# Optimization experiments

Hardware: AMD Instinct MI355X
Metric: run time of the kernel (lower is better)

## Reference

```python
import jax, jax.numpy as jnp
import numpy as np

EMBED_DIM = 1024
NUM_HEADS = 16
HEAD_DIM = EMBED_DIM // NUM_HEADS
THRESHOLD = 0.001
B, S = 8, 1024


def setup_inputs() -> dict:
    key = jax.random.key(0)
    ks = jax.random.split(key, 7)
    sc = 1.0 / np.sqrt(EMBED_DIM)
    return {
        "x": jax.random.normal(ks[0], (B, S, EMBED_DIM), dtype=jnp.float32),
        "Wq": jax.random.normal(ks[1], (NUM_HEADS, EMBED_DIM, HEAD_DIM), dtype=jnp.float32) * sc,
        "bq": jax.random.normal(ks[2], (NUM_HEADS, HEAD_DIM), dtype=jnp.float32) * 0.01,
        "Wk": jax.random.normal(ks[3], (NUM_HEADS, EMBED_DIM, HEAD_DIM), dtype=jnp.float32) * sc,
        "bk": jax.random.normal(ks[4], (NUM_HEADS, HEAD_DIM), dtype=jnp.float32) * 0.01,
        "Wv": jax.random.normal(ks[5], (NUM_HEADS, EMBED_DIM, HEAD_DIM), dtype=jnp.float32) * sc,
        "bv": jax.random.normal(ks[6], (NUM_HEADS, HEAD_DIM), dtype=jnp.float32) * 0.01,
    }


def thresholded_softmax(scores, threshold):
    # softmax over last dim, zero entries below threshold, renormalize
    s = jax.nn.softmax(scores, axis=-1)
    s = jnp.where(s < threshold, 0.0, s)
    return s / (jnp.sum(s, axis=-1, keepdims=True) + 1e-12)


def reference(x, Wq, bq, Wk, bk, Wv, bv):
    # x: [B,S,D]; Wq/Wk/Wv: [H,D,e]; biases: [H,e]
    scale = jnp.asarray(EMBED_DIM ** 0.5, x.dtype)  # note: scales by sqrt(embed_dim), not head_dim
    Q = jnp.einsum("bsd,hde->hbse", x, Wq) + bq[:, None, None, :]
    K = jnp.einsum("bsd,hde->hbse", x, Wk) + bk[:, None, None, :]
    V = jnp.einsum("bsd,hde->hbse", x, Wv) + bv[:, None, None, :]
    scores = jnp.einsum("hbse,hbte->hbst", Q, K) / scale  # [H,B,S,S]
    att = thresholded_softmax(scores, THRESHOLD)
    latent = jnp.einsum("hbst,hbte->hbse", att, V)  # [H,B,S,e]
    # concat heads along last dim in head order -> [B,S,H*e]
    residual = jnp.transpose(latent, (1, 2, 0, 3)).reshape(x.shape[0], x.shape[1], -1)
    x_res = x + residual  # dropout p=0.0 -> identity
    return (x_res, att)
```

## Files before the change

### kernel.cpp

```cpp
#include <hip/hip_runtime.h>
#include <hip/hip_bf16.h>
#include <cstdint>
#include <cstddef>

#define B_ 8
#define S_ 1024
#define H_ 16
#define E_ 64
#define D_ 1024

typedef unsigned short u16;
typedef short s16x8 __attribute__((ext_vector_type(8)));
typedef float f32x4 __attribute__((ext_vector_type(4)));

__device__ __forceinline__ u16 f2b(float f) {
  union { float f; unsigned u; } v; v.f = f;
  unsigned u = v.u;
  return (u16)((u + 0x7FFFu + ((u >> 16) & 1u)) >> 16);
}

__device__ __forceinline__ void gload16(const void* g, void* lds) {
  __builtin_amdgcn_global_load_lds(
      (const __attribute__((address_space(1))) void*)g,
      (__attribute__((address_space(3))) void*)lds, 16, 0, 0);
}

#define BARL() do {                                          \
  asm volatile("s_waitcnt lgkmcnt(0)" ::: "memory");         \
  __builtin_amdgcn_sched_barrier(0);                         \
  __builtin_amdgcn_s_barrier();                              \
  __builtin_amdgcn_sched_barrier(0);                         \
  asm volatile("" ::: "memory");                             \
} while (0)

__global__ void k_prep(const float* __restrict__ x, u16* __restrict__ xb,
                       const float* __restrict__ Wq, const float* __restrict__ Wk,
                       const float* __restrict__ Wv, u16* __restrict__ wbt) {
  if (blockIdx.x < 4096) {
    size_t i = ((size_t)blockIdx.x * 256 + threadIdx.x) * 8;
    float4 a = *(const float4*)(x + i);
    float4 b = *(const float4*)(x + i + 4);
    uint4 o;
    o.x = f2b(a.x) | ((unsigned)f2b(a.y) << 16);
    o.y = f2b(a.z) | ((unsigned)f2b(a.w) << 16);
    o.z = f2b(b.x) | ((unsigned)f2b(b.y) << 16);
    o.w = f2b(b.z) | ((unsigned)f2b(b.w) << 16);
    *(uint4*)(xb + i) = o;
    return;
  }
  __shared__ u16 T[64][65];
  int bid = blockIdx.x - 4096;
  int d0 = (bid & 15) * 64;
  int mh = bid >> 4;
  int mat = mh >> 4, h = mh & 15;
  const float* W = (mat == 0) ? Wq : (mat == 1) ? Wk : Wv;
  int tid = threadIdx.x;
#pragma unroll
  for (int rep = 0; rep < 4; rep++) {
    int dl = rep * 16 + (tid >> 4);
    int e0 = (tid & 15) * 4;
    float4 v = *(const float4*)(W + (size_t)h * (D_ * E_) + (size_t)(d0 + dl) * E_ + e0);
    T[dl][e0] = f2b(v.x); T[dl][e0 + 1] = f2b(v.y);
    T[dl][e0 + 2] = f2b(v.z); T[dl][e0 + 3] = f2b(v.w);
  }
  __syncthreads();
#pragma unroll
  for (int rep = 0; rep < 4; rep++) {
    int el = rep * 16 + (tid >> 4);
    int dl0 = (tid & 15) * 4;
    ushort4 o;
    o.x = T[dl0][el]; o.y = T[dl0 + 1][el]; o.z = T[dl0 + 2][el]; o.w = T[dl0 + 3][el];
    int n = mat * 1024 + h * 64 + el;
    *(ushort4*)(wbt + (size_t)n * D_ + d0 + dl0) = o;
  }
}

__global__ __launch_bounds__(256) void k_qkv(
    const u16* __restrict__ xb, const u16* __restrict__ wbt,
    const float* __restrict__ bq, const float* __restrict__ bk, const float* __restrict__ bv,
    u16* __restrict__ Qb, u16* __restrict__ Kb, u16* __restrict__ Vt) {
  __shared__ u16 As[128 * 64];
  __shared__ u16 Bs[128 * 64];
  int tid = threadIdx.x, l = tid & 63, w = tid >> 6;
  int bid = blockIdx.x;
  int xcd = bid & 7, i = bid >> 3;
  int m0 = (xcd * 8 + i / 24) * 128;
  int n0 = (i % 24) * 128;
  int wm = w >> 1, wn = w & 1;
  int rl = l & 15, kg = l >> 4;
  f32x4 acc[4][4] = {};
  for (int k0 = 0; k0 < D_; k0 += 64) {
#pragma unroll
    for (int i2 = 0; i2 < 4; i2++) {
      int ci = w * 4 + i2;
      int r = ci * 8 + (l >> 3);
      int c = (l & 7) ^ (r & 7);
      gload16(xb  + (size_t)(m0 + r) * D_ + k0 + c * 8, (char*)As + ci * 1024);
      gload16(wbt + (size_t)(n0 + r) * D_ + k0 + c * 8, (char*)Bs + ci * 1024);
    }
    __syncthreads();
#pragma unroll
    for (int kk = 0; kk < 2; kk++) {
      s16x8 af[4], bfr[4];
      int chunk = kk * 4 + kg;
#pragma unroll
      for (int fm = 0; fm < 4; fm++) {
        int r = wm * 64 + fm * 16 + rl;
        af[fm] = *(const s16x8*)(As + r * 64 + ((chunk ^ (r & 7)) * 8));
      }
#pragma unroll
      for (int fn = 0; fn < 4; fn++) {
        int r = wn * 64 + fn * 16 + rl;
        bfr[fn] = *(const s16x8*)(Bs + r * 64 + ((chunk ^ (r & 7)) * 8));
      }
#pragma unroll
      for (int fm = 0; fm < 4; fm++)
#pragma unroll
        for (int fn = 0; fn < 4; fn++)
          acc[fm][fn] = __builtin_amdgcn_mfma_f32_16x16x32_bf16(af[fm], bfr[fn], acc[fm][fn], 0, 0, 0);
    }
    __syncthreads();
  }
#pragma unroll
  for (int fn = 0; fn < 4; fn++) {
    int n = n0 + wn * 64 + fn * 16 + rl;
    int mat = n >> 10, h = (n >> 6) & 15, e = n & 63;
    const float* bias = (mat == 0) ? bq : (mat == 1) ? bk : bv;
    float bval = bias[h * 64 + e];
    if (mat == 2) {
#pragma unroll
      for (int fm = 0; fm < 4; fm++) {
        int sq = m0 + wm * 64 + fm * 16 + kg * 4;
        int bb = sq >> 10, s = sq & 1023;
        ushort4 o;
        o.x = f2b(acc[fm][fn][0] + bval);
        o.y = f2b(acc[fm][fn][1] + bval);
        o.z = f2b(acc[fm][fn][2] + bval);
        o.w = f2b(acc[fm][fn][3] + bval);
        *(ushort4*)(Vt + ((size_t)((h * B_ + bb) * E_ + e) << 10) + s) = o;
      }
    } else {
      u16* dst = (mat == 0) ? Qb : Kb;
#pragma unroll
      for (int fm = 0; fm < 4; fm++)
#pragma unroll
        for (int j = 0; j < 4; j++) {
          int m = m0 + wm * 64 + fm * 16 + kg * 4 + j;
          int bb = m >> 10, s = m & 1023;
          dst[(size_t)((h * B_ + bb) * S_ + s) * E_ + e] = f2b(acc[fm][fn][j] + bval);
        }
    }
  }
}

__global__ __launch_bounds__(512, 2) void f_attn(
    const u16* __restrict__ Qb, const u16* __restrict__ Kb, const u16* __restrict__ Vt,
    const float* __restrict__ x, float* __restrict__ att, float* __restrict__ out) {
  __shared__ u16 Qlds[64 * 64];
  __shared__ u16 KV[1024 * 64];
  __shared__ u16 Ab[2][64 * 64];
  __shared__ float red[3][64][4];

  int p = blockIdx.x;
  int L = (p & 7) * 256 + (p >> 3);
  int hb = L >> 4, mblk = L & 15;
  int m0 = mblk * 64;
  int tid = threadIdx.x, l = tid & 63, w = tid >> 6;
  int rl = l & 15, kg = l >> 4;
  int rh = w >> 2, cq = w & 3;

  const u16* Qp = Qb + (size_t)hb * (S_ * E_) + (size_t)m0 * E_;
  const u16* Kp = Kb + (size_t)hb * (S_ * E_);
  const u16* Vp = Vt + (size_t)hb * (S_ * E_);

  {
    int r = w * 8 + (l >> 3), c = (l & 7) ^ (r & 7);
    gload16(Qp + (size_t)r * E_ + c * 8, (char*)Qlds + w * 1024);
  }
#pragma unroll
  for (int i = 0; i < 16; i++) {
    int ci = w * 16 + i;
    int r = ci * 8 + (l >> 3), c = (l & 7) ^ (r & 7);
    gload16(Kp + (size_t)r * E_ + c * 8, (char*)KV + ci * 1024);
  }
  __syncthreads();

  s16x8 af[2][2];
#pragma unroll
  for (int fm = 0; fm < 2; fm++)
#pragma unroll
    for (int kk = 0; kk < 2; kk++) {
      int r = rh * 32 + fm * 16 + rl, ch = kk * 4 + kg;
      af[fm][kk] = *(const s16x8*)((const char*)Qlds + r * 128 + ((ch ^ (r & 7)) * 16));
    }

  f32x4 acc[2][16];
#pragma unroll
  for (int fm = 0; fm < 2; fm++)
#pragma unroll
    for (int ct = 0; ct < 16; ct++)
#pragma unroll
      for (int j = 0; j < 4; j++) acc[fm][ct][j] = 0.f;

#pragma unroll
  for (int ct = 0; ct < 16; ct++) {
    s16x8 bf[2];
#pragma unroll
    for (int kk = 0; kk < 2; kk++) {
      int r = ct * 64 + cq * 16 + rl, ch = kk * 4 + kg;
      bf[kk] = *(const s16x8*)((const char*)KV + r * 128 + ((ch ^ (r & 7)) * 16));
    }
#pragma unroll
    for (int fm = 0; fm < 2; fm++)
#pragma unroll
      for (int kk = 0; kk < 2; kk++)
        acc[fm][ct] = __builtin_amdgcn_mfma_f32_16x16x32_bf16(af[fm][kk], bf[kk], acc[fm][ct], 0, 0, 0);
  }
  __syncthreads();

#pragma unroll
  for (int i = 0; i < 16; i++) {
    int ci = w * 16 + i;
    int e = ci >> 1, hf = ci & 1;
    int c = ((hf * 64 + l) & ~7) | ((l & 7) ^ (e & 7));
    gload16(Vp + (size_t)e * S_ + c * 8, (char*)KV + e * 2048 + hf * 1024);
  }

  int mh2 = w >> 1, nh2 = w & 1;
  int h = hb >> 3, bb = hb & 7;
  float xv[2][4];
#pragma unroll
  for (int fn = 0; fn < 2; fn++)
#pragma unroll
    for (int j = 0; j < 4; j++) {
      int mq = m0 + mh2 * 16 + kg * 4 + j;
      int e = h * 64 + nh2 * 32 + fn * 16 + rl;
      xv[fn][j] = x[(((size_t)bb * S_ + mq) << 10) + e];
    }

  float mx[2][4], Z[2][4], Z2[2][4];
#pragma unroll
  for (int fm = 0; fm < 2; fm++)
#pragma unroll
    for (int j = 0; j < 4; j++) {
      float m = acc[fm][0][j];
#pragma unroll
      for (int ct = 1; ct < 16; ct++) m = fmaxf(m, acc[fm][ct][j]);
#pragma unroll
      for (int off = 8; off >= 1; off >>= 1) m = fmaxf(m, __shfl_xor(m, off));
      mx[fm][j] = m;
    }
  if (rl == 0) {
#pragma unroll
    for (int fm = 0; fm < 2; fm++)
#pragma unroll
      for (int j = 0; j < 4; j++) red[0][rh * 32 + fm * 16 + kg * 4 + j][cq] = mx[fm][j];
  }
  BARL();
#pragma unroll
  for (int fm = 0; fm < 2; fm++)
#pragma unroll
    for (int j = 0; j < 4; j++) {
      f32x4 r4 = *(const f32x4*)&red[0][rh * 32 + fm * 16 + kg * 4 + j][0];
      mx[fm][j] = fmaxf(fmaxf(r4[0], r4[1]), fmaxf(r4[2], r4[3]));
    }
#pragma unroll
  for (int fm = 0; fm < 2; fm++)
#pragma unroll
    for (int j = 0; j < 4; j++) {
      float s = 0.f;
#pragma unroll
      for (int ct = 0; ct < 16; ct++) {
        float e = __expf((acc[fm][ct][j] - mx[fm][j]) * 0.03125f);
        acc[fm][ct][j] = e;
        s += e;
      }
#pragma unroll
      for (int off = 8; off >= 1; off >>= 1) s += __shfl_xor(s, off);
      Z[fm][j] = s;
    }
  if (rl == 0) {
#pragma unroll
    for (int fm = 0; fm < 2; fm++)
#pragma unroll
      for (int j = 0; j < 4; j++) red[1][rh * 32 + fm * 16 + kg * 4 + j][cq] = Z[fm][j];
  }
  BARL();
#pragma unroll
  for (int fm = 0; fm < 2; fm++)
#pragma unroll
    for (int j = 0; j < 4; j++) {
      f32x4 r4 = *(const f32x4*)&red[1][rh * 32 + fm * 16 + kg * 4 + j][0];
      Z[fm][j] = r4[0] + r4[1] + r4[2] + r4[3];
    }
#pragma unroll
  for (int fm = 0; fm < 2; fm++)
#pragma unroll
    for (int j = 0; j < 4; j++) {
      float thr = 0.001f * Z[fm][j];
      float s = 0.f;
#pragma unroll
      for (int ct = 0; ct < 16; ct++) {
        float e = acc[fm][ct][j];
        e = (e >= thr) ? e : 0.f;
        acc[fm][ct][j] = e;
        s += e;
      }
#pragma unroll
      for (int off = 8; off >= 1; off >>= 1) s += __shfl_xor(s, off);
      Z2[fm][j] = s;
    }
  if (rl == 0) {
#pragma unroll
    for (int fm = 0; fm < 2; fm++)
#pragma unroll
      for (int j = 0; j < 4; j++) red[2][rh * 32 + fm * 16 + kg * 4 + j][cq] = Z2[fm][j];
  }
  BARL();
#pragma unroll
  for (int fm = 0; fm < 2; fm++)
#pragma unroll
    for (int j = 0; j < 4; j++) {
      f32x4 r4 = *(const f32x4*)&red[2][rh * 32 + fm * 16 + kg * 4 + j][0];
      float z2 = r4[0] + r4[1] + r4[2] + r4[3];
      float inv = 1.f / (z2 + 1e-12f * Z[fm][j]);
#pragma unroll
      for (int ct = 0; ct < 16; ct++) acc[fm][ct][j] *= inv;
    }

  asm volatile("s_waitcnt vmcnt(0)" ::: "memory");
  __builtin_amdgcn_sched_barrier(0);

  float* attp = att + ((size_t)hb << 20) + ((size_t)m0 << 10);
#pragma unroll
  for (int fm = 0; fm < 2; fm++)
#pragma unroll
    for (int j = 0; j < 4; j++) {
      int m = rh * 32 + fm * 16 + kg * 4 + j;
#pragma unroll
      for (int ct = 0; ct < 16; ct++)
        attp[((size_t)m << 10) + ct * 64 + cq * 16 + rl] = acc[fm][ct][j];
    }

  f32x4 acc2[2];
#pragma unroll
  for (int fn = 0; fn < 2; fn++)
#pragma unroll
    for (int j = 0; j < 4; j++) acc2[fn][j] = 0.f;

#pragma unroll
  for (int fm = 0; fm < 2; fm++)
#pragma unroll
    for (int j = 0; j < 4; j++) {
      int m = rh * 32 + fm * 16 + kg * 4 + j;
      int tl = cq * 16 + rl;
      *(u16*)((char*)Ab[0] + m * 128 + (((tl >> 3) ^ (m & 7)) * 16) + (tl & 7) * 2)
          = f2b(acc[fm][0][j]);
    }
  BARL();

#pragma unroll
  for (int ct = 0; ct < 16; ct++) {
    s16x8 a2[2], b2[2][2];
#pragma unroll
    for (int kk = 0; kk < 2; kk++) {
      int ch = kk * 4 + kg;
      int rA = mh2 * 16 + rl;
      a2[kk] = *(const s16x8*)((const char*)Ab[ct & 1] + rA * 128 + ((ch ^ (rA & 7)) * 16));
#pragma unroll
      for (int fn = 0; fn < 2; fn++) {
        int e = nh2 * 32 + fn * 16 + rl;
        b2[fn][kk] = *(const s16x8*)((const char*)KV + e * 2048 + ct * 128 + ((ch ^ (e & 7)) * 16));
      }
    }
    if (ct < 15) {
#pragma unroll
      for (int fm = 0; fm < 2; fm++)
#pragma unroll
        for (int j = 0; j < 4; j++) {
          int m = rh * 32 + fm * 16 + kg * 4 + j;
          int tl = cq * 16 + rl;
          *(u16*)((char*)Ab[(ct + 1) & 1] + m * 128 + (((tl >> 3) ^ (m & 7)) * 16) + (tl & 7) * 2)
              = f2b(acc[fm][ct + 1][j]);
        }
    }
    __builtin_amdgcn_s_setprio(1);
#pragma unroll
    for (int fn = 0; fn < 2; fn++)
#pragma unroll
      for (int kk = 0; kk < 2; kk++)
        acc2[fn] = __builtin_amdgcn_mfma_f32_16x16x32_bf16(a2[kk], b2[fn][kk], acc2[fn], 0, 0, 0);
    __builtin_amdgcn_s_setprio(0);
    BARL();
  }

#pragma unroll
  for (int fn = 0; fn < 2; fn++)
#pragma unroll
    for (int j = 0; j < 4; j++) {
      int mq = m0 + mh2 * 16 + kg * 4 + j;
      int e = h * 64 + nh2 * 32 + fn * 16 + rl;
      size_t idx = (((size_t)bb * S_ + mq) << 10) + e;
      out[idx] = xv[fn][j] + acc2[fn][j];
    }
}

extern "C" void kernel_launch(void* const* d_in, const int* in_sizes, int n_in,
                              void* d_out, int out_size, void* d_ws, size_t ws_size,
                              hipStream_t stream) {
  const float* x  = (const float*)d_in[0];
  const float* Wq = (const float*)d_in[1];
  const float* bq = (const float*)d_in[2];
  const float* Wk = (const float*)d_in[3];
  const float* bk = (const float*)d_in[4];
  const float* Wv = (const float*)d_in[5];
  const float* bv = (const float*)d_in[6];
  float* xres = (float*)d_out;
  float* att  = xres + (size_t)B_ * S_ * D_;

  char* ws = (char*)d_ws;
  u16* xb  = (u16*)(ws);
  u16* wbt = (u16*)(ws + 16777216);
  u16* Qb  = (u16*)(ws + 23068672);
  u16* Kb  = (u16*)(ws + 39845888);
  u16* Vt  = (u16*)(ws + 56623104);

  k_prep  <<<dim3(4864), dim3(256), 0, stream>>>(x, xb, Wq, Wk, Wv, wbt);
  k_qkv   <<<dim3(1536), dim3(256), 0, stream>>>(xb, wbt, bq, bk, bv, Qb, Kb, Vt);
  f_attn  <<<dim3(2048), dim3(512), 0, stream>>>(Qb, Kb, Vt, x, att, xres);
}
```

Before: 287.9 us.

## Shrink attention tile to 32 rows and stream K/V in halves

The attention kernel now processes 32 query rows per block with 4 waves (256 threads) instead of 64 rows with 8 waves. It loads K and V in two 512-column halves into a smaller LDS buffer, which cuts LDS use so more blocks can be resident per CU. It also moves the att write after the PV loop and doubles the grid. In exchange, each block re-reads K/V from global or L2 twice as often per query row, and the extra sync points on the half-loads can stall.

```diff
diff --git a/kernel.cpp b/kernel.cpp
--- a/kernel.cpp
+++ b/kernel.cpp
@@ -153,21 +153,20 @@
   }
 }
 
-__global__ __launch_bounds__(512, 2) void f_attn(
+__global__ __launch_bounds__(256, 2) void f_attn(
     const u16* __restrict__ Qb, const u16* __restrict__ Kb, const u16* __restrict__ Vt,
     const float* __restrict__ x, float* __restrict__ att, float* __restrict__ out) {
-  __shared__ u16 Qlds[64 * 64];
-  __shared__ u16 KV[1024 * 64];
-  __shared__ u16 Ab[2][64 * 64];
-  __shared__ float red[3][64][4];
+  __shared__ u16 KV[512 * 64];
+  __shared__ u16 Ab[2][32 * 64];
+  __shared__ u16 Qlds[32 * 64];
+  __shared__ float red[3][32][4];
 
   int p = blockIdx.x;
-  int L = (p & 7) * 256 + (p >> 3);
-  int hb = L >> 4, mblk = L & 15;
-  int m0 = mblk * 64;
+  int L = (p & 7) * 512 + (p >> 3);
+  int hb = L >> 5, mblk = L & 31;
+  int m0 = mblk * 32;
   int tid = threadIdx.x, l = tid & 63, w = tid >> 6;
   int rl = l & 15, kg = l >> 4;
-  int rh = w >> 2, cq = w & 3;
 
   const u16* Qp = Qb + (size_t)hb * (S_ * E_) + (size_t)m0 * E_;
   const u16* Kp = Kb + (size_t)hb * (S_ * E_);
@@ -190,8 +189,8 @@
   for (int fm = 0; fm < 2; fm++)
 #pragma unroll
     for (int kk = 0; kk < 2; kk++) {
-      int r = rh * 32 + fm * 16 + rl, ch = kk * 4 + kg;
-      af[fm][kk] = *(const s16x8*)((const char*)Qlds + r * 128 + ((ch ^ (r & 7)) * 16));
+      int q = fm * 16 + rl, ch = kk * 4 + kg;
+      af[fm][kk] = *(const s16x8*)((const char*)Qlds + q * 128 + ((ch ^ (q & 7)) * 16));
     }
 
   f32x4 acc[2][16];
@@ -203,11 +202,11 @@
       for (int j = 0; j < 4; j++) acc[fm][ct][j] = 0.f;
 
 #pragma unroll
-  for (int ct = 0; ct < 16; ct++) {
+  for (int ct = 0; ct < 8; ct++) {
     s16x8 bf[2];
 #pragma unroll
     for (int kk = 0; kk < 2; kk++) {
-      int r = ct * 64 + cq * 16 + rl, ch = kk * 4 + kg;
+      int r = ct * 64 + w * 16 + rl, ch = kk * 4 + kg;
       bf[kk] = *(const s16x8*)((const char*)KV + r * 128 + ((ch ^ (r & 7)) * 16));
     }
 #pragma unroll
@@ -216,26 +215,48 @@
       for (int kk = 0; kk < 2; kk++)
         acc[fm][ct] = __builtin_amdgcn_mfma_f32_16x16x32_bf16(af[fm][kk], bf[kk], acc[fm][ct], 0, 0, 0);
   }
-  __syncthreads();
+  BARL();
 
 #pragma unroll
   for (int i = 0; i < 16; i++) {
     int ci = w * 16 + i;
-    int e = ci >> 1, hf = ci & 1;
-    int c = ((hf * 64 + l) & ~7) | ((l & 7) ^ (e & 7));
-    gload16(Vp + (size_t)e * S_ + c * 8, (char*)KV + e * 2048 + hf * 1024);
-  }
-
-  int mh2 = w >> 1, nh2 = w & 1;
+    int r = ci * 8 + (l >> 3), c = (l & 7) ^ (r & 7);
+    gload16(Kp + (size_t)(512 + r) * E_ + c * 8, (char*)KV + ci * 1024);
+  }
+  __syncthreads();
+
+#pragma unroll
+  for (int ct = 0; ct < 8; ct++) {
+    s16x8 bf[2];
+#pragma unroll
+    for (int kk = 0; kk < 2; kk++) {
+      int r = ct * 64 + w * 16 + rl, ch = kk * 4 + kg;
+      bf[kk] = *(const s16x8*)((const char*)KV + r * 128 + ((ch ^ (r & 7)) * 16));
+    }
+#pragma unroll
+    for (int fm = 0; fm < 2; fm++)
+#pragma unroll
+      for (int kk = 0; kk < 2; kk++)
+        acc[fm][8 + ct] = __builtin_amdgcn_mfma_f32_16x16x32_bf16(af[fm][kk], bf[kk], acc[fm][8 + ct], 0, 0, 0);
+  }
+  BARL();
+
+#pragma unroll
+  for (int i = 0; i < 16; i++) {
+    int e = w * 16 + i;
+    int c = (l & ~7) | ((l & 7) ^ (e & 7));
+    gload16(Vp + (size_t)e * S_ + c * 8, (char*)KV + e * 1024);
+  }
+
   int h = hb >> 3, bb = hb & 7;
   float xv[2][4];
 #pragma unroll
-  for (int fn = 0; fn < 2; fn++)
-#pragma unroll
-    for (int j = 0; j < 4; j++) {
-      int mq = m0 + mh2 * 16 + kg * 4 + j;
-      int e = h * 64 + nh2 * 32 + fn * 16 + rl;
-      xv[fn][j] = x[(((size_t)bb * S_ + mq) << 10) + e];
+  for (int fm = 0; fm < 2; fm++)
+#pragma unroll
+    for (int j = 0; j < 4; j++) {
+      int mq = m0 + fm * 16 + kg * 4 + j;
+      int e = h * 64 + w * 16 + rl;
+      xv[fm][j] = x[(((size_t)bb * S_ + mq) << 10) + e];
     }
 
   float mx[2][4], Z[2][4], Z2[2][4];
@@ -254,14 +275,14 @@
 #pragma unroll
     for (int fm = 0; fm < 2; fm++)
 #pragma unroll
-      for (int j = 0; j < 4; j++) red[0][rh * 32 + fm * 16 + kg * 4 + j][cq] = mx[fm][j];
-  }
-  BARL();
-#pragma unroll
-  for (int fm = 0; fm < 2; fm++)
-#pragma unroll
-    for (int j = 0; j < 4; j++) {
-      f32x4 r4 = *(const f32x4*)&red[0][rh * 32 + fm * 16 + kg * 4 + j][0];
+      for (int j = 0; j < 4; j++) red[0][fm * 16 + kg * 4 + j][w] = mx[fm][j];
+  }
+  BARL();
+#pragma unroll
+  for (int fm = 0; fm < 2; fm++)
+#pragma unroll
+    for (int j = 0; j < 4; j++) {
+      f32x4 r4 = *(const f32x4*)&red[0][fm * 16 + kg * 4 + j][0];
       mx[fm][j] = fmaxf(fmaxf(r4[0], r4[1]), fmaxf(r4[2], r4[3]));
     }
 #pragma unroll
@@ -283,14 +304,14 @@
 #pragma unroll
     for (int fm = 0; fm < 2; fm++)
 #pragma unroll
-      for (int j = 0; j < 4; j++) red[1][rh * 32 + fm * 16 + kg * 4 + j][cq] = Z[fm][j];
-  }
-  BARL();
-#pragma unroll
-  for (int fm = 0; fm < 2; fm++)
-#pragma unroll
-    for (int j = 0; j < 4; j++) {
-      f32x4 r4 = *(const f32x4*)&red[1][rh * 32 + fm * 16 + kg * 4 + j][0];
+      for (int j = 0; j < 4; j++) red[1][fm * 16 + kg * 4 + j][w] = Z[fm][j];
+  }
+  BARL();
+#pragma unroll
+  for (int fm = 0; fm < 2; fm++)
+#pragma unroll
+    for (int j = 0; j < 4; j++) {
+      f32x4 r4 = *(const f32x4*)&red[1][fm * 16 + kg * 4 + j][0];
       Z[fm][j] = r4[0] + r4[1] + r4[2] + r4[3];
     }
 #pragma unroll
@@ -314,14 +335,14 @@
 #pragma unroll
     for (int fm = 0; fm < 2; fm++)
 #pragma unroll
-      for (int j = 0; j < 4; j++) red[2][rh * 32 + fm * 16 + kg * 4 + j][cq] = Z2[fm][j];
-  }
-  BARL();
-#pragma unroll
-  for (int fm = 0; fm < 2; fm++)
-#pragma unroll
-    for (int j = 0; j < 4; j++) {
-      f32x4 r4 = *(const f32x4*)&red[2][rh * 32 + fm * 16 + kg * 4 + j][0];
+      for (int j = 0; j < 4; j++) red[2][fm * 16 + kg * 4 + j][w] = Z2[fm][j];
+  }
+  BARL();
+#pragma unroll
+  for (int fm = 0; fm < 2; fm++)
+#pragma unroll
+    for (int j = 0; j < 4; j++) {
+      f32x4 r4 = *(const f32x4*)&red[2][fm * 16 + kg * 4 + j][0];
       float z2 = r4[0] + r4[1] + r4[2] + r4[3];
       float inv = 1.f / (z2 + 1e-12f * Z[fm][j]);
 #pragma unroll
@@ -331,46 +352,37 @@
   asm volatile("s_waitcnt vmcnt(0)" ::: "memory");
   __builtin_amdgcn_sched_barrier(0);
 
-  float* attp = att + ((size_t)hb << 20) + ((size_t)m0 << 10);
-#pragma unroll
-  for (int fm = 0; fm < 2; fm++)
-#pragma unroll
-    for (int j = 0; j < 4; j++) {
-      int m = rh * 32 + fm * 16 + kg * 4 + j;
-#pragma unroll
-      for (int ct = 0; ct < 16; ct++)
-        attp[((size_t)m << 10) + ct * 64 + cq * 16 + rl] = acc[fm][ct][j];
-    }
-
-  f32x4 acc2[2];
-#pragma unroll
-  for (int fn = 0; fn < 2; fn++)
-#pragma unroll
-    for (int j = 0; j < 4; j++) acc2[fn][j] = 0.f;
-
-#pragma unroll
-  for (int fm = 0; fm < 2; fm++)
-#pragma unroll
-    for (int j = 0; j < 4; j++) {
-      int m = rh * 32 + fm * 16 + kg * 4 + j;
-      int tl = cq * 16 + rl;
+#pragma unroll
+  for (int fm = 0; fm < 2; fm++)
+#pragma unroll
+    for (int j = 0; j < 4; j++) {
+      int m = fm * 16 + kg * 4 + j;
+      int tl = w * 16 + rl;
       *(u16*)((char*)Ab[0] + m * 128 + (((tl >> 3) ^ (m & 7)) * 16) + (tl & 7) * 2)
           = f2b(acc[fm][0][j]);
     }
   BARL();
 
+  f32x4 acc2[2];
+#pragma unroll
+  for (int fm = 0; fm < 2; fm++)
+#pragma unroll
+    for (int j = 0; j < 4; j++) acc2[fm][j] = 0.f;
+
 #pragma unroll
   for (int ct = 0; ct < 16; ct++) {
-    s16x8 a2[2], b2[2][2];
+    s16x8 a2[2][2], b2[2];
 #pragma unroll
     for (int kk = 0; kk < 2; kk++) {
       int ch = kk * 4 + kg;
-      int rA = mh2 * 16 + rl;
-      a2[kk] = *(const s16x8*)((const char*)Ab[ct & 1] + rA * 128 + ((ch ^ (rA & 7)) * 16));
-#pragma unroll
-      for (int fn = 0; fn < 2; fn++) {
-        int e = nh2 * 32 + fn * 16 + rl;
-        b2[fn][kk] = *(const s16x8*)((const char*)KV + e * 2048 + ct * 128 + ((ch ^ (e & 7)) * 16));
+#pragma unroll
+      for (int fm = 0; fm < 2; fm++) {
+        int rA = fm * 16 + rl;
+        a2[fm][kk] = *(const s16x8*)((const char*)Ab[ct & 1] + rA * 128 + ((ch ^ (rA & 7)) * 16));
+      }
+      {
+        int e = w * 16 + rl;
+        b2[kk] = *(const s16x8*)((const char*)KV + e * 1024 + (ct & 7) * 128 + ((ch ^ (e & 7)) * 16));
       }
     }
     if (ct < 15) {
@@ -378,30 +390,52 @@
       for (int fm = 0; fm < 2; fm++)
 #pragma unroll
         for (int j = 0; j < 4; j++) {
-          int m = rh * 32 + fm * 16 + kg * 4 + j;
-          int tl = cq * 16 + rl;
+          int m = fm * 16 + kg * 4 + j;
+          int tl = w * 16 + rl;
           *(u16*)((char*)Ab[(ct + 1) & 1] + m * 128 + (((tl >> 3) ^ (m & 7)) * 16) + (tl & 7) * 2)
               = f2b(acc[fm][ct + 1][j]);
         }
     }
     __builtin_amdgcn_s_setprio(1);
 #pragma unroll
-    for (int fn = 0; fn < 2; fn++)
+    for (int fm = 0; fm < 2; fm++)
 #pragma unroll
       for (int kk = 0; kk < 2; kk++)
-        acc2[fn] = __builtin_amdgcn_mfma_f32_16x16x32_bf16(a2[kk], b2[fn][kk], acc2[fn], 0, 0, 0);
+        acc2[fm] = __builtin_amdgcn_mfma_f32_16x16x32_bf16(a2[fm][kk], b2[kk], acc2[fm], 0, 0, 0);
     __builtin_amdgcn_s_setprio(0);
     BARL();
-  }
-
-#pragma unroll
-  for (int fn = 0; fn < 2; fn++)
-#pragma unroll
-    for (int j = 0; j < 4; j++) {
-      int mq = m0 + mh2 * 16 + kg * 4 + j;
-      int e = h * 64 + nh2 * 32 + fn * 16 + rl;
+    if (ct == 7) {
+#pragma unroll
+      for (int i = 0; i < 16; i++) {
+        int e = w * 16 + i;
+        int c = (l & ~7) | ((l & 7) ^ (e & 7));
+        gload16(Vp + (size_t)e * S_ + 512 + c * 8, (char*)KV + e * 1024);
+      }
+      asm volatile("s_waitcnt vmcnt(0)" ::: "memory");
+      __builtin_amdgcn_sched_barrier(0);
+      BARL();
+    }
+  }
+
+  float* attp = att + ((size_t)hb << 20) + ((size_t)m0 << 10);
+#pragma unroll
+  for (int fm = 0; fm < 2; fm++)
+#pragma unroll
+    for (int j = 0; j < 4; j++) {
+      int m = fm * 16 + kg * 4 + j;
+#pragma unroll
+      for (int ct = 0; ct < 16; ct++)
+        attp[((size_t)m << 10) + ct * 64 + w * 16 + rl] = acc[fm][ct][j];
+    }
+
+#pragma unroll
+  for (int fm = 0; fm < 2; fm++)
+#pragma unroll
+    for (int j = 0; j < 4; j++) {
+      int mq = m0 + fm * 16 + kg * 4 + j;
+      int e = h * 64 + w * 16 + rl;
       size_t idx = (((size_t)bb * S_ + mq) << 10) + e;
-      out[idx] = xv[fn][j] + acc2[fn][j];
+      out[idx] = xv[fm][j] + acc2[fm][j];
     }
 }
 
@@ -427,5 +461,5 @@
 
   k_prep  <<<dim3(4864), dim3(256), 0, stream>>>(x, xb, Wq, Wk, Wv, wbt);
   k_qkv   <<<dim3(1536), dim3(256), 0, stream>>>(xb, wbt, bq, bk, bv, Qb, Kb, Vt);
-  f_attn  <<<dim3(2048), dim3(512), 0, stream>>>(Qb, Kb, Vt, x, att, xres);
-}
+  f_attn  <<<dim3(4096), dim3(256), 0, stream>>>(Qb, Kb, Vt, x, att, xres);
+}
```

Result: slower. 344.5 us (+19.7%).
